# Kernel tuning notes

Measured on AMD Instinct MI355X. Metric: run time of the kernel, lower is better.

## Reference

```python
import jax, jax.numpy as jnp
import numpy as np


def setup_inputs() -> dict:
    key = jax.random.key(0)
    kq, kk, kv, km = jax.random.split(key, 4)
    B, H, S, D = 2, 16, 2048, 64
    Q = jax.random.normal(kq, (B, H, S, D), dtype=jnp.float32)
    K = jax.random.normal(kk, (B, H, S, D), dtype=jnp.float32)
    V = jax.random.normal(kv, (B, H, S, D), dtype=jnp.float32)
    attn_mask = jax.random.randint(km, (B, 1, S, S), 0, 2).astype(jnp.bool_)
    return {"Q": Q, "K": K, "V": V, "attn_mask": attn_mask}


def reference(Q, K, V, attn_mask):
    d_k = Q.shape[-1]
    # scores = Q @ K^T / sqrt(d_k)  -> [B, H, S, S]
    scores = jnp.einsum('bhqd,bhkd->bhqk', Q, K) / jnp.sqrt(jnp.float32(d_k))
    # faithful to torch masked_fill_(attn_mask, 1e-9): masked positions set to 1e-9
    scores = jnp.where(attn_mask, jnp.float32(1e-9), scores)
    attn = jax.nn.softmax(scores, axis=-1)
    context = jnp.einsum('bhqk,bhkd->bhqd', attn, V)
    return (context, attn)
```

## Files before the change

### kernel.cpp

```cpp
#include <hip/hip_runtime.h>

#define BB 2
#define HH 16
#define SS 2048
#define DD 64

typedef __attribute__((ext_vector_type(8))) _Float16 half8;
typedef __attribute__((ext_vector_type(4))) float f32x4;
typedef __attribute__((ext_vector_type(4))) unsigned int u32x4;

__device__ __forceinline__ half8 cvt8(f32x4 a, f32x4 b) {
  half8 r;
  r[0] = (_Float16)a[0]; r[1] = (_Float16)a[1];
  r[2] = (_Float16)a[2]; r[3] = (_Float16)a[3];
  r[4] = (_Float16)b[0]; r[5] = (_Float16)b[1];
  r[6] = (_Float16)b[2]; r[7] = (_Float16)b[3];
  return r;
}

__global__ __launch_bounds__(512, 4)
void sdpa_kernel(const float* __restrict__ Q, const float* __restrict__ K,
                 const float* __restrict__ V, const void* __restrict__ M,
                 float* __restrict__ out_ctx, float* __restrict__ out_attn) {
  __shared__ _Float16 E[16 * 2048];
  __shared__ unsigned int mbits[16][64];
  __shared__ float zacc[8][16];
  __shared__ f32x4 pscr[4][64];

  const int bh   = blockIdx.y;
  const int b    = bh >> 4;
  const int q0   = blockIdx.x << 4;
  const int tid  = threadIdx.x;
  const int wave = tid >> 6;
  const int lane = tid & 63;
  const int col  = lane & 15;
  const int quad = lane >> 4;

  const unsigned int* mw = (const unsigned int*)M;
  unsigned int probe = mw[lane];
  unsigned long long bi = __ballot(probe <= 1u);
  unsigned long long bf = __ballot(probe == 0u || probe == 0x3f800000u);
  const int mmode = (bi == ~0ull) ? 0 : ((bf == ~0ull) ? 1 : 2);

  const float* Qb = Q + (size_t)bh * SS * DD;
  const float* Kb = K + (size_t)bh * SS * DD;
  const float* Vb = V + (size_t)bh * SS * DD;

  half8 aQ0, aQ1;
  {
    const float* qp = Qb + (size_t)(q0 + col) * DD + quad * 8;
    f32x4 x0 = *(const f32x4*)(qp);
    f32x4 x1 = *(const f32x4*)(qp + 4);
    f32x4 x2 = *(const f32x4*)(qp + 32);
    f32x4 x3 = *(const f32x4*)(qp + 36);
    aQ0 = cvt8(x0, x1);
    aQ1 = cvt8(x2, x3);
  }

  {
    unsigned int* mflat = &mbits[0][0];
    mflat[tid] = 0u;
    mflat[tid + 512] = 0u;
    __syncthreads();
    if (mmode == 2) {
      const unsigned char* mb = (const unsigned char*)M + (size_t)b * SS * SS + (size_t)q0 * SS;
#pragma unroll
      for (int j = 0; j < 4; ++j) {
        const int lin = (tid + j * 512) * 16;
        u32x4 v = *(const u32x4*)(mb + lin);
        unsigned int bits = 0;
#pragma unroll
        for (int w = 0; w < 4; ++w) {
          unsigned int x = v[w];
          bits |= ((x & 0x000000ffu) ? 1u : 0u) << (w * 4 + 0);
          bits |= ((x & 0x0000ff00u) ? 1u : 0u) << (w * 4 + 1);
          bits |= ((x & 0x00ff0000u) ? 1u : 0u) << (w * 4 + 2);
          bits |= ((x & 0xff000000u) ? 1u : 0u) << (w * 4 + 3);
        }
        const int row = lin >> 11, key0 = lin & 2047;
        atomicOr(&mbits[row][key0 >> 5], bits << (key0 & 31));
      }
    } else {
      const unsigned int* mv4 = (const unsigned int*)M + (size_t)b * SS * SS + (size_t)q0 * SS;
#pragma unroll
      for (int j = 0; j < 16; ++j) {
        const int lin = (tid + j * 512) * 4;
        u32x4 v = *(const u32x4*)(mv4 + lin);
        unsigned int bits = 0;
        bits |= v[0] ? 1u : 0u;
        bits |= v[1] ? 2u : 0u;
        bits |= v[2] ? 4u : 0u;
        bits |= v[3] ? 8u : 0u;
        const int row = lin >> 11, key0 = lin & 2047;
        atomicOr(&mbits[row][key0 >> 5], bits << (key0 & 31));
      }
    }
    __syncthreads();
  }

  float zpart[4] = {0.f, 0.f, 0.f, 0.f};
#pragma unroll 4
  for (int n0 = wave * 16; n0 < SS; n0 += 128) {
    const float* kp = Kb + (size_t)(n0 + col) * DD + quad * 8;
    f32x4 x0 = *(const f32x4*)(kp);
    f32x4 x1 = *(const f32x4*)(kp + 4);
    f32x4 x2 = *(const f32x4*)(kp + 32);
    f32x4 x3 = *(const f32x4*)(kp + 36);
    half8 bK0 = cvt8(x0, x1);
    half8 bK1 = cvt8(x2, x3);
    f32x4 c = {0.f, 0.f, 0.f, 0.f};
    c = __builtin_amdgcn_mfma_f32_16x16x32_f16(aQ0, bK0, c, 0, 0, 0);
    c = __builtin_amdgcn_mfma_f32_16x16x32_f16(aQ1, bK1, c, 0, 0, 0);
    const int key    = n0 + col;
    const int mword  = n0 >> 5;
    const int mshift = (n0 & 16) + col;
#pragma unroll
    for (int r = 0; r < 4; ++r) {
      const int row = quad * 4 + r;
      const int mv = (mbits[row][mword] >> mshift) & 1;
      const float sc = mv ? 1e-9f : c[r] * 0.125f;
      const float e  = __expf(sc);
      zpart[r] += e;
      const int gp = (key >> 3) ^ (row & 7);
      E[row * 2048 + gp * 8 + (key & 7)] = (_Float16)e;
    }
  }
#pragma unroll
  for (int r = 0; r < 4; ++r) {
    float z = zpart[r];
    z += __shfl_xor(z, 1, 64);
    z += __shfl_xor(z, 2, 64);
    z += __shfl_xor(z, 4, 64);
    z += __shfl_xor(z, 8, 64);
    if (col == 0) zacc[wave][quad * 4 + r] = z;
  }
  __syncthreads();

  const int d0 = (wave & 3) << 4;
  const int h  = wave >> 2;
  const int kbase = h << 10;
  float rzr[2];
#pragma unroll
  for (int rr = 0; rr < 2; ++rr) {
    const int row = (wave << 1) + rr;
    float z = 0.f;
#pragma unroll
    for (int w = 0; w < 8; ++w) z += zacc[w][row];
    rzr[rr] = 1.0f / z;
  }
  f32x4 u = {0.f, 0.f, 0.f, 0.f};
#pragma unroll 4
  for (int t = 0; t < 32; ++t) {
    const int kk0 = kbase + t * 32;
    const int gp = ((kk0 + quad * 8) >> 3) ^ (col & 7);
    half8 aP = *(const half8*)&E[col * 2048 + gp * 8];
    const float* vp = Vb + (size_t)(kk0 + quad * 8) * DD + d0 + col;
    half8 bV;
#pragma unroll
    for (int jj = 0; jj < 8; ++jj) bV[jj] = (_Float16)vp[(size_t)jj * DD];
    u = __builtin_amdgcn_mfma_f32_16x16x32_f16(aP, bV, u, 0, 0, 0);
    if ((t & 3) == 3) {
      const int g   = t >> 2;
      const int rr  = g >> 2;
      const int i   = g & 3;
      const int row = (wave << 1) + rr;
      const int gpr = i * 64 + lane;
      half8 v = *(const half8*)&E[row * 2048 + gpr * 8];
      const int gcol = i * 64 + (lane ^ (row & 7));
      float* arow = out_attn + ((size_t)bh * SS + (q0 + row)) * SS;
      f32x4 w0, w1;
#pragma unroll
      for (int j = 0; j < 4; ++j) {
        w0[j] = (float)v[j] * rzr[rr];
        w1[j] = (float)v[j + 4] * rzr[rr];
      }
      *(f32x4*)(arow + gcol * 8)     = w0;
      *(f32x4*)(arow + gcol * 8 + 4) = w1;
    }
  }
  if (h) pscr[wave & 3][lane] = u;
  __syncthreads();

  if (h == 0) {
    f32x4 u2 = pscr[wave][lane];
#pragma unroll
    for (int r = 0; r < 4; ++r) {
      const int row = quad * 4 + r;
      float z = 0.f;
#pragma unroll
      for (int w = 0; w < 8; ++w) z += zacc[w][row];
      out_ctx[((size_t)bh * SS + (q0 + row)) * DD + d0 + col] = (u[r] + u2[r]) / z;
    }
  }
}

extern "C" void kernel_launch(void* const* d_in, const int* in_sizes, int n_in,
                              void* d_out, int out_size, void* d_ws, size_t ws_size,
                              hipStream_t stream) {
  const float* Q = (const float*)d_in[0];
  const float* K = (const float*)d_in[1];
  const float* V = (const float*)d_in[2];
  const void*  M = d_in[3];
  float* ctx  = (float*)d_out;
  float* attn = ctx + (size_t)BB * HH * SS * DD;
  dim3 grid(SS / 16, BB * HH);
  sdpa_kernel<<<grid, 512, 0, stream>>>(Q, K, V, M, ctx, attn);
}
```

Before: 965.5 us.

## Pre-convert K/V to fp16 in workspace and halve query rows per block

Adds a pre-pass kernel that converts K and V to fp16 in the workspace, so the attention kernel reads half the bytes and skips per-block conversion. Query rows per block drop from 16 to 8, which doubles the grid and raises the occupancy hint. Half of each MFMA's output rows are now discarded, so every block still does a full 16-row Q·K^T while keeping only 8 rows. K/V reads across all blocks double in count, though they are now fp16. The mask bit array is padded to 68 words per row, likely to reduce LDS bank conflicts.

```diff
diff --git a/kernel.cpp b/kernel.cpp
--- a/kernel.cpp
+++ b/kernel.cpp
@@ -4,8 +4,10 @@
 #define HH 16
 #define SS 2048
 #define DD 64
+#define QR 8
 
 typedef __attribute__((ext_vector_type(8))) _Float16 half8;
+typedef __attribute__((ext_vector_type(4))) _Float16 half4;
 typedef __attribute__((ext_vector_type(4))) float f32x4;
 typedef __attribute__((ext_vector_type(4))) unsigned int u32x4;
 
@@ -18,18 +20,36 @@
   return r;
 }
 
-__global__ __launch_bounds__(512, 4)
+__global__ __launch_bounds__(256, 8)
+void cvt_kv(const float* __restrict__ K, const float* __restrict__ V,
+            _Float16* __restrict__ K16, _Float16* __restrict__ V16) {
+  const size_t N4 = (size_t)BB * HH * SS * DD / 4;
+  for (size_t i = (size_t)blockIdx.x * blockDim.x + threadIdx.x; i < N4;
+       i += (size_t)gridDim.x * blockDim.x) {
+    f32x4 k = *((const f32x4*)K + i);
+    f32x4 v = *((const f32x4*)V + i);
+    half4 kh, vh;
+#pragma unroll
+    for (int j = 0; j < 4; ++j) { kh[j] = (_Float16)k[j]; vh[j] = (_Float16)v[j]; }
+    *((half4*)K16 + i) = kh;
+    *((half4*)V16 + i) = vh;
+  }
+}
+
+template <bool F16>
+__global__ __launch_bounds__(512, 8)
 void sdpa_kernel(const float* __restrict__ Q, const float* __restrict__ K,
                  const float* __restrict__ V, const void* __restrict__ M,
+                 const _Float16* __restrict__ K16g, const _Float16* __restrict__ V16g,
                  float* __restrict__ out_ctx, float* __restrict__ out_attn) {
-  __shared__ _Float16 E[16 * 2048];
-  __shared__ unsigned int mbits[16][64];
-  __shared__ float zacc[8][16];
+  __shared__ _Float16 E[QR * 2048];
+  __shared__ unsigned int mbits[QR][68];
+  __shared__ float zacc[8][QR];
   __shared__ f32x4 pscr[4][64];
 
   const int bh   = blockIdx.y;
   const int b    = bh >> 4;
-  const int q0   = blockIdx.x << 4;
+  const int q0   = blockIdx.x * QR;
   const int tid  = threadIdx.x;
   const int wave = tid >> 6;
   const int lane = tid & 63;
@@ -45,10 +65,12 @@
   const float* Qb = Q + (size_t)bh * SS * DD;
   const float* Kb = K + (size_t)bh * SS * DD;
   const float* Vb = V + (size_t)bh * SS * DD;
+  const _Float16* K16b = K16g + (size_t)bh * SS * DD;
+  const _Float16* V16b = V16g + (size_t)bh * SS * DD;
 
   half8 aQ0, aQ1;
   {
-    const float* qp = Qb + (size_t)(q0 + col) * DD + quad * 8;
+    const float* qp = Qb + (size_t)(q0 + (col & 7)) * DD + quad * 8;
     f32x4 x0 = *(const f32x4*)(qp);
     f32x4 x1 = *(const f32x4*)(qp + 4);
     f32x4 x2 = *(const f32x4*)(qp + 32);
@@ -59,13 +81,12 @@
 
   {
     unsigned int* mflat = &mbits[0][0];
-    mflat[tid] = 0u;
-    mflat[tid + 512] = 0u;
+    for (int i = tid; i < QR * 68; i += 512) mflat[i] = 0u;
     __syncthreads();
     if (mmode == 2) {
       const unsigned char* mb = (const unsigned char*)M + (size_t)b * SS * SS + (size_t)q0 * SS;
 #pragma unroll
-      for (int j = 0; j < 4; ++j) {
+      for (int j = 0; j < 2; ++j) {
         const int lin = (tid + j * 512) * 16;
         u32x4 v = *(const u32x4*)(mb + lin);
         unsigned int bits = 0;
@@ -83,7 +104,7 @@
     } else {
       const unsigned int* mv4 = (const unsigned int*)M + (size_t)b * SS * SS + (size_t)q0 * SS;
 #pragma unroll
-      for (int j = 0; j < 16; ++j) {
+      for (int j = 0; j < 8; ++j) {
         const int lin = (tid + j * 512) * 4;
         u32x4 v = *(const u32x4*)(mv4 + lin);
         unsigned int bits = 0;
@@ -99,30 +120,39 @@
   }
 
   float zpart[4] = {0.f, 0.f, 0.f, 0.f};
-#pragma unroll 4
+#pragma unroll 2
   for (int n0 = wave * 16; n0 < SS; n0 += 128) {
-    const float* kp = Kb + (size_t)(n0 + col) * DD + quad * 8;
-    f32x4 x0 = *(const f32x4*)(kp);
-    f32x4 x1 = *(const f32x4*)(kp + 4);
-    f32x4 x2 = *(const f32x4*)(kp + 32);
-    f32x4 x3 = *(const f32x4*)(kp + 36);
-    half8 bK0 = cvt8(x0, x1);
-    half8 bK1 = cvt8(x2, x3);
+    half8 bK0, bK1;
+    if (F16) {
+      const _Float16* kp = K16b + (size_t)(n0 + col) * DD + quad * 8;
+      bK0 = *(const half8*)(kp);
+      bK1 = *(const half8*)(kp + 32);
+    } else {
+      const float* kp = Kb + (size_t)(n0 + col) * DD + quad * 8;
+      f32x4 x0 = *(const f32x4*)(kp);
+      f32x4 x1 = *(const f32x4*)(kp + 4);
+      f32x4 x2 = *(const f32x4*)(kp + 32);
+      f32x4 x3 = *(const f32x4*)(kp + 36);
+      bK0 = cvt8(x0, x1);
+      bK1 = cvt8(x2, x3);
+    }
     f32x4 c = {0.f, 0.f, 0.f, 0.f};
     c = __builtin_amdgcn_mfma_f32_16x16x32_f16(aQ0, bK0, c, 0, 0, 0);
     c = __builtin_amdgcn_mfma_f32_16x16x32_f16(aQ1, bK1, c, 0, 0, 0);
     const int key    = n0 + col;
     const int mword  = n0 >> 5;
     const int mshift = (n0 & 16) + col;
-#pragma unroll
-    for (int r = 0; r < 4; ++r) {
-      const int row = quad * 4 + r;
-      const int mv = (mbits[row][mword] >> mshift) & 1;
-      const float sc = mv ? 1e-9f : c[r] * 0.125f;
-      const float e  = __expf(sc);
-      zpart[r] += e;
-      const int gp = (key >> 3) ^ (row & 7);
-      E[row * 2048 + gp * 8 + (key & 7)] = (_Float16)e;
+    if (quad < 2) {
+#pragma unroll
+      for (int r = 0; r < 4; ++r) {
+        const int row = quad * 4 + r;
+        const int mv = (mbits[row][mword] >> mshift) & 1;
+        const float sc = mv ? 1e-9f : c[r] * 0.125f;
+        const float e  = __expf(sc);
+        zpart[r] += e;
+        const int gp = (key >> 3) ^ row;
+        E[row * 2048 + gp * 8 + (key & 7)] = (_Float16)e;
+      }
     }
   }
 #pragma unroll
@@ -132,47 +162,49 @@
     z += __shfl_xor(z, 2, 64);
     z += __shfl_xor(z, 4, 64);
     z += __shfl_xor(z, 8, 64);
-    if (col == 0) zacc[wave][quad * 4 + r] = z;
+    if (quad < 2 && col == 0) zacc[wave][quad * 4 + r] = z;
   }
   __syncthreads();
 
   const int d0 = (wave & 3) << 4;
   const int h  = wave >> 2;
   const int kbase = h << 10;
-  float rzr[2];
-#pragma unroll
-  for (int rr = 0; rr < 2; ++rr) {
-    const int row = (wave << 1) + rr;
+  float rz;
+  {
     float z = 0.f;
 #pragma unroll
-    for (int w = 0; w < 8; ++w) z += zacc[w][row];
-    rzr[rr] = 1.0f / z;
+    for (int w = 0; w < 8; ++w) z += zacc[w][wave];
+    rz = 1.0f / z;
   }
   f32x4 u = {0.f, 0.f, 0.f, 0.f};
 #pragma unroll 4
   for (int t = 0; t < 32; ++t) {
     const int kk0 = kbase + t * 32;
     const int gp = ((kk0 + quad * 8) >> 3) ^ (col & 7);
-    half8 aP = *(const half8*)&E[col * 2048 + gp * 8];
-    const float* vp = Vb + (size_t)(kk0 + quad * 8) * DD + d0 + col;
+    half8 aP = *(const half8*)&E[(col & 7) * 2048 + gp * 8];
     half8 bV;
-#pragma unroll
-    for (int jj = 0; jj < 8; ++jj) bV[jj] = (_Float16)vp[(size_t)jj * DD];
+    if (F16) {
+      const _Float16* vp = V16b + (size_t)(kk0 + quad * 8) * DD + d0 + col;
+#pragma unroll
+      for (int jj = 0; jj < 8; ++jj) bV[jj] = vp[(size_t)jj * DD];
+    } else {
+      const float* vp = Vb + (size_t)(kk0 + quad * 8) * DD + d0 + col;
+#pragma unroll
+      for (int jj = 0; jj < 8; ++jj) bV[jj] = (_Float16)vp[(size_t)jj * DD];
+    }
     u = __builtin_amdgcn_mfma_f32_16x16x32_f16(aP, bV, u, 0, 0, 0);
-    if ((t & 3) == 3) {
-      const int g   = t >> 2;
-      const int rr  = g >> 2;
-      const int i   = g & 3;
-      const int row = (wave << 1) + rr;
+    if ((t & 7) == 7) {
+      const int i   = t >> 3;
+      const int row = wave;
       const int gpr = i * 64 + lane;
       half8 v = *(const half8*)&E[row * 2048 + gpr * 8];
-      const int gcol = i * 64 + (lane ^ (row & 7));
+      const int gcol = i * 64 + (lane ^ row);
       float* arow = out_attn + ((size_t)bh * SS + (q0 + row)) * SS;
       f32x4 w0, w1;
 #pragma unroll
       for (int j = 0; j < 4; ++j) {
-        w0[j] = (float)v[j] * rzr[rr];
-        w1[j] = (float)v[j + 4] * rzr[rr];
+        w0[j] = (float)v[j] * rz;
+        w1[j] = (float)v[j + 4] * rz;
       }
       *(f32x4*)(arow + gcol * 8)     = w0;
       *(f32x4*)(arow + gcol * 8 + 4) = w1;
@@ -183,13 +215,15 @@
 
   if (h == 0) {
     f32x4 u2 = pscr[wave][lane];
-#pragma unroll
-    for (int r = 0; r < 4; ++r) {
-      const int row = quad * 4 + r;
-      float z = 0.f;
-#pragma unroll
-      for (int w = 0; w < 8; ++w) z += zacc[w][row];
-      out_ctx[((size_t)bh * SS + (q0 + row)) * DD + d0 + col] = (u[r] + u2[r]) / z;
+    if (quad < 2) {
+#pragma unroll
+      for (int r = 0; r < 4; ++r) {
+        const int row = quad * 4 + r;
+        float z = 0.f;
+#pragma unroll
+        for (int w = 0; w < 8; ++w) z += zacc[w][row];
+        out_ctx[((size_t)bh * SS + (q0 + row)) * DD + d0 + col] = (u[r] + u2[r]) / z;
+      }
     }
   }
 }
@@ -203,6 +237,14 @@
   const void*  M = d_in[3];
   float* ctx  = (float*)d_out;
   float* attn = ctx + (size_t)BB * HH * SS * DD;
-  dim3 grid(SS / 16, BB * HH);
-  sdpa_kernel<<<grid, 512, 0, stream>>>(Q, K, V, M, ctx, attn);
-}
+  dim3 grid(SS / QR, BB * HH);
+  const size_t nkv = (size_t)BB * HH * SS * DD;
+  if (ws_size >= 2 * nkv * sizeof(_Float16) && d_ws != nullptr) {
+    _Float16* K16 = (_Float16*)d_ws;
+    _Float16* V16 = K16 + nkv;
+    cvt_kv<<<dim3(2048), 256, 0, stream>>>(K, V, K16, V16);
+    sdpa_kernel<true><<<grid, 512, 0, stream>>>(Q, K, V, M, K16, V16, ctx, attn);
+  } else {
+    sdpa_kernel<false><<<grid, 512, 0, stream>>>(Q, K, V, M, nullptr, nullptr, ctx, attn);
+  }
+}
```

After: 964.0 us. About the same (-0.2%).
